# Performance work log

Measured on AMD Instinct MI355X. Metric: run time of the kernel, lower is better.

The kernel has to match this reference:

```python
import jax, jax.numpy as jnp
import numpy as np

B, C, H, W = 8, 256, 64, 64
CR = C // 8  # reduced channels = 32


def setup_inputs() -> dict:
    key = jax.random.key(0)
    k1, k2, k3, k4 = jax.random.split(key, 4)
    x = jax.random.normal(k1, (B, C, H, W), dtype=jnp.float32)
    # 1x1 conv weights (bias=False) are plain channel matmuls; scale like kaiming (~1/sqrt(fan_in))
    Wt = jax.random.normal(k2, (3 * CR, C), dtype=jnp.float32) * (1.0 / np.sqrt(C))
    Wo = jax.random.normal(k3, (C, CR), dtype=jnp.float32) * (1.0 / np.sqrt(CR))
    scale = jax.random.normal(k4, (1,), dtype=jnp.float32)
    return {"x": x, "Wt": Wt, "Wo": Wo, "scale": scale}


def reference(x, Wt, Wo, scale):
    b, c, h, w = x.shape
    n = h * w
    # 1x1 conv QKV projection: [B, 3*Cr, H, W]
    t = jnp.einsum('oc,bchw->bohw', Wt, x)
    cr = t.shape[1] // 3
    key = t[:, :cr].reshape(b, cr, n)          # [B, Cr, N]
    query = t[:, cr:2 * cr].reshape(b, cr, n)  # [B, Cr, N]
    value = t[:, 2 * cr:].reshape(b, cr, n)    # [B, Cr, N]
    # scores[b, i, j] = sum_c key[b,c,i] * query[b,c,j]  (key^T @ query)
    scores = jnp.einsum('bci,bcj->bij', key, query)  # [B, N, N]
    # torch Softmax(dim=1): normalize over the key axis i
    weights = jax.nn.softmax(scores, axis=1)
    # output[b, c, j] = sum_i value[b,c,i] * weights[b,i,j]
    out = jnp.einsum('bci,bij->bcj', value, weights)  # [B, Cr, N]
    out = out.reshape(b, cr, h, w)
    out = jnp.einsum('oc,bchw->bohw', Wo, out)  # 1x1 conv back to C channels
    return scale[0] * out + x
```

## Files before the change

### kernel.cpp

```cpp
#include <hip/hip_runtime.h>
#include <math.h>

#define B_ 8
#define C_ 256
#define CR_ 32
#define N_ 4096
#define NH_ 4

typedef __attribute__((ext_vector_type(8))) short bf16x8;
typedef __attribute__((ext_vector_type(4))) short bf16x4;
typedef __attribute__((ext_vector_type(4))) float f32x4;
typedef __attribute__((ext_vector_type(16))) float f32x16;
typedef __attribute__((ext_vector_type(2))) unsigned uint32x2;

#if defined(__has_builtin)
#if __has_builtin(__builtin_amdgcn_permlane32_swap)
#define HAVE_PLSWAP 1
#endif
#endif

__device__ inline short f2bf(float f) {
  union { float f; unsigned u; } v; v.f = f;
  unsigned r = v.u + 0x7FFFu + ((v.u >> 16) & 1u);
  return (short)(r >> 16);
}
__device__ inline float bf2f(short h) {
  union { unsigned u; float f; } v; v.u = ((unsigned)(unsigned short)h) << 16;
  return v.f;
}
__device__ inline short f2bf_r(float f) {
  return (short)((__float_as_uint(f) + 0x8000u) >> 16);
}


__global__ __launch_bounds__(256) void prep_weights(const float* __restrict__ Wt,
                                                    const float* __restrict__ Wo,
                                                    const float* __restrict__ scale,
                                                    short* __restrict__ WtHi,
                                                    short* __restrict__ WtLo,
                                                    short* __restrict__ WoB) {
  const int blk = blockIdx.x, tid = threadIdx.x;
  if (blk < 96) {
    float v = Wt[blk * C_ + tid];
    if (blk >= 32 && blk < 64) v *= 1.44269504f;
    const short h = f2bf(v);
    WtHi[blk * C_ + tid] = h;
    WtLo[blk * C_ + tid] = f2bf(v - bf2f(h));
  } else {
    const int idx = (blk - 96) * 256 + tid;
    WoB[idx] = f2bf(Wo[idx] * scale[0]);
  }
}

__global__ __launch_bounds__(256) void qkv_mfma(const float* __restrict__ x,
                                                const short* __restrict__ WtHi,
                                                const short* __restrict__ WtLo,
                                                short* __restrict__ Kf,
                                                short* __restrict__ Qf,
                                                short* __restrict__ Vf) {
  const int b = blockIdx.y;
  const int tid = threadIdx.x;
  const int wave = tid >> 6, lane = tid & 63;
  const int col = lane & 15, quad = lane >> 4;
  const int n0 = (blockIdx.x * 4 + wave) * 16;

  const f32x4 z4 = {0.f, 0.f, 0.f, 0.f};
  f32x4 acc[6] = {z4, z4, z4, z4, z4, z4};

  const float* xb = x + (size_t)b * C_ * N_ + n0 + col;
  float xcur[8], xnxt[8];
#pragma unroll
  for (int j = 0; j < 8; ++j) xcur[j] = xb[(size_t)(quad * 8 + j) * N_];

#pragma unroll 2
  for (int c0 = 0; c0 < C_; c0 += 32) {
    if (c0 < C_ - 32) {
#pragma unroll
      for (int j = 0; j < 8; ++j)
        xnxt[j] = xb[(size_t)(c0 + 32 + quad * 8 + j) * N_];
    }
    bf16x8 xh, xl;
#pragma unroll
    for (int j = 0; j < 8; ++j) {
      const short h = (short)(__float_as_uint(xcur[j]) >> 16);
      xh[j] = h;
      xl[j] = f2bf_r(xcur[j] - bf2f(h));
    }
#pragma unroll
    for (int ot = 0; ot < 4; ++ot) {
      const int off = (ot * 16 + col) * C_ + c0 + quad * 8;
      const bf16x8 bh = *(const bf16x8*)(WtHi + off);
      const bf16x8 bl = *(const bf16x8*)(WtLo + off);
      acc[ot] = __builtin_amdgcn_mfma_f32_16x16x32_bf16(xh, bh, acc[ot], 0, 0, 0);
      acc[ot] = __builtin_amdgcn_mfma_f32_16x16x32_bf16(xl, bh, acc[ot], 0, 0, 0);
      acc[ot] = __builtin_amdgcn_mfma_f32_16x16x32_bf16(xh, bl, acc[ot], 0, 0, 0);
    }
#pragma unroll
    for (int ct = 0; ct < 2; ++ct) {
      const int off = ((64 + ct * 16) + col) * C_ + c0 + quad * 8;
      const bf16x8 ah = *(const bf16x8*)(WtHi + off);
      const bf16x8 al = *(const bf16x8*)(WtLo + off);
      acc[4 + ct] = __builtin_amdgcn_mfma_f32_16x16x32_bf16(ah, xh, acc[4 + ct], 0, 0, 0);
      acc[4 + ct] = __builtin_amdgcn_mfma_f32_16x16x32_bf16(ah, xl, acc[4 + ct], 0, 0, 0);
      acc[4 + ct] = __builtin_amdgcn_mfma_f32_16x16x32_bf16(al, xh, acc[4 + ct], 0, 0, 0);
    }
#pragma unroll
    for (int j = 0; j < 8; ++j) xcur[j] = xnxt[j];
  }

#pragma unroll
  for (int ot = 0; ot < 2; ++ot)
#pragma unroll
    for (int r = 0; r < 4; ++r) {
      const int i = n0 + quad * 4 + r;
      const int c = ot * 16 + col;
      const int ln = (i & 31) | (((c >> 3) & 1) << 5);
      Kf[(((size_t)(b * 128 + (i >> 5)) * 2 + (c >> 4)) * 64 + ln) * 8 + (c & 7)] =
          f2bf(acc[ot][r]);
    }
#pragma unroll
  for (int ot = 2; ot < 4; ++ot)
#pragma unroll
    for (int r = 0; r < 4; ++r) {
      const int j = n0 + quad * 4 + r;
      const int c = (ot - 2) * 16 + col;
      const int ln = (j & 31) | (((c >> 3) & 1) << 5);
      Qf[(((size_t)(b * 128 + (j >> 5)) * 2 + (c >> 4)) * 64 + ln) * 8 + (c & 7)] =
          f2bf(acc[ot][r]);
    }
#pragma unroll
  for (int ct = 0; ct < 2; ++ct)
#pragma unroll
    for (int r = 0; r < 4; ++r) {
      const int c = ct * 16 + quad * 4 + r;
      const int n = n0 + col;
      const int ln = c | (((n >> 3) & 1) << 5);
      Vf[((size_t)(b * 256 + (n >> 4)) * 64 + ln) * 8 + (n & 7)] =
          f2bf(acc[4 + ct][r]);
    }
}

__global__ __launch_bounds__(64, 2) void flash_attn(const short* __restrict__ Kf,
                                                    const short* __restrict__ Qf,
                                                    const short* __restrict__ Vf,
                                                    short* __restrict__ OPart,
                                                    float* __restrict__ LPart) {
  const int b = blockIdx.z, hq = blockIdx.y;
  const int jb = blockIdx.x;
  const int lane = threadIdx.x;
  const int j32 = lane & 31, h32 = lane >> 5;

  const f32x16 z16 = {0.f};
  const short* pQ = Qf + ((size_t)(b * 128 + jb * 2) * 2) * 512 + lane * 8;
  bf16x8 qf[2][2];
  qf[0][0] = *(const bf16x8*)(pQ);
  qf[0][1] = *(const bf16x8*)(pQ + 512);
  qf[1][0] = *(const bf16x8*)(pQ + 1024);
  qf[1][1] = *(const bf16x8*)(pQ + 1536);

  const short* pK = Kf + ((size_t)(b * 128 + hq * 32) * 2) * 512 + lane * 8;
  const short* pV = Vf + ((size_t)(b * 256 + hq * 64)) * 512 + lane * 8;

  f32x16 acc[2] = {z16, z16};
  float ps[2] = {0.f, 0.f};

  bf16x8 ka = *(const bf16x8*)(pK);
  bf16x8 kb = *(const bf16x8*)(pK + 512);
  bf16x8 va = *(const bf16x8*)(pV);
  bf16x8 vb = *(const bf16x8*)(pV + 512);

#pragma unroll 1
  for (int t = 0; t < 32; ++t) {
    pK += 1024;
    pV += 1024;
    const bf16x8 kan = *(const bf16x8*)(pK);
    const bf16x8 kbn = *(const bf16x8*)(pK + 512);
    const bf16x8 van = *(const bf16x8*)(pV);
    const bf16x8 vbn = *(const bf16x8*)(pV + 512);

#pragma unroll
    for (int jt = 0; jt < 2; ++jt) {
      __builtin_amdgcn_s_setprio(1);
      f32x16 s = __builtin_amdgcn_mfma_f32_32x32x16_bf16(ka, qf[jt][0], z16, 0, 0, 0);
      s = __builtin_amdgcn_mfma_f32_32x32x16_bf16(kb, qf[jt][1], s, 0, 0, 0);
      __builtin_amdgcn_s_setprio(0);
      float p[16];
#pragma unroll
      for (int r = 0; r < 16; ++r) p[r] = __builtin_amdgcn_exp2f(s[r]);
      ps[jt] += (((p[0] + p[1]) + (p[2] + p[3])) + ((p[4] + p[5]) + (p[6] + p[7]))) +
                (((p[8] + p[9]) + (p[10] + p[11])) + ((p[12] + p[13]) + (p[14] + p[15])));
      unsigned d[8];
#pragma unroll
      for (int k = 0; k < 8; ++k) {
        const unsigned u0 = __float_as_uint(p[2 * k]) + 0x8000u;
        const unsigned u1 = __float_as_uint(p[2 * k + 1]) + 0x8000u;
        d[k] = __builtin_amdgcn_perm(u1, u0, 0x07060302u);
      }
      union { unsigned u[4]; bf16x8 v; } f0, f1;
#ifdef HAVE_PLSWAP
      {
        const uint32x2 r0 = __builtin_amdgcn_permlane32_swap(d[0], d[2], false, false);
        f0.u[0] = r0[0]; f0.u[2] = r0[1];
        const uint32x2 r1 = __builtin_amdgcn_permlane32_swap(d[1], d[3], false, false);
        f0.u[1] = r1[0]; f0.u[3] = r1[1];
        const uint32x2 r2 = __builtin_amdgcn_permlane32_swap(d[4], d[6], false, false);
        f1.u[0] = r2[0]; f1.u[2] = r2[1];
        const uint32x2 r3 = __builtin_amdgcn_permlane32_swap(d[5], d[7], false, false);
        f1.u[1] = r3[0]; f1.u[3] = r3[1];
      }
#else
      {
        unsigned xw[8];
#pragma unroll
        for (int k = 0; k < 8; ++k) xw[k] = __shfl_xor((int)d[k], 32);
        f0.u[0] = h32 ? xw[2] : d[0];
        f0.u[1] = h32 ? xw[3] : d[1];
        f0.u[2] = h32 ? d[2] : xw[0];
        f0.u[3] = h32 ? d[3] : xw[1];
        f1.u[0] = h32 ? xw[6] : d[4];
        f1.u[1] = h32 ? xw[7] : d[5];
        f1.u[2] = h32 ? d[6] : xw[4];
        f1.u[3] = h32 ? d[7] : xw[5];
      }
#endif
      __builtin_amdgcn_s_setprio(1);
      acc[jt] = __builtin_amdgcn_mfma_f32_32x32x16_bf16(va, f0.v, acc[jt], 0, 0, 0);
      acc[jt] = __builtin_amdgcn_mfma_f32_32x32x16_bf16(vb, f1.v, acc[jt], 0, 0, 0);
      __builtin_amdgcn_s_setprio(0);
    }

    ka = kan; kb = kbn; va = van; vb = vbn;
  }

  const size_t base = ((size_t)b * NH_ + hq) * N_;
#pragma unroll
  for (int jt = 0; jt < 2; ++jt) {
    const float l = ps[jt] + __shfl_xor(ps[jt], 32);
    const int jg = (jb * 2 + jt) * 32 + j32;
    if (h32 == 0) LPart[base + jg] = l;
    short* OP = OPart + (base + jg) * 32;
#pragma unroll
    for (int g = 0; g < 4; ++g) {
      bf16x4 o = {f2bf(acc[jt][4 * g + 0]), f2bf(acc[jt][4 * g + 1]),
                  f2bf(acc[jt][4 * g + 2]), f2bf(acc[jt][4 * g + 3])};
      *(bf16x4*)(OP + 8 * g + 4 * h32) = o;
    }
  }
}

__global__ __launch_bounds__(256) void out_proj(const short* __restrict__ OPart,
                                                const float* __restrict__ LPart,
                                                const short* __restrict__ WoB,
                                                const float* __restrict__ x,
                                                float* __restrict__ out) {
  const int b = blockIdx.z, chalf = blockIdx.y;
  const int tid = threadIdx.x;
  const int wave = tid >> 6, lane = tid & 63;
  const int col = lane & 15, quad = lane >> 4;
  const int jg = blockIdx.x * 64 + wave * 16 + col;
  const int n0 = blockIdx.x * 64 + wave * 16;

  float osum[8];
#pragma unroll
  for (int e = 0; e < 8; ++e) osum[e] = 0.f;
  float lsum = 0.f;
#pragma unroll
  for (int h = 0; h < NH_; ++h) {
    const size_t p = ((size_t)b * NH_ + h) * N_ + jg;
    const bf16x8 o = *(const bf16x8*)(OPart + p * 32 + quad * 8);
#pragma unroll
    for (int e = 0; e < 8; ++e) osum[e] += bf2f(o[e]);
    lsum += LPart[p];
  }
  const float linv = 1.f / lsum;
  bf16x8 bf;
#pragma unroll
  for (int e = 0; e < 8; ++e) bf[e] = f2bf(osum[e] * linv);

  const f32x4 z4 = {0.f, 0.f, 0.f, 0.f};
  const float* xb = x + (size_t)b * C_ * N_;
  float* ob = out + (size_t)b * C_ * N_;
#pragma unroll
  for (int ct = 0; ct < 8; ++ct) {
    const int ctg = chalf * 8 + ct;
    const bf16x8 af = *(const bf16x8*)(WoB + (ctg * 16 + col) * 32 + quad * 8);
    const f32x4 a = __builtin_amdgcn_mfma_f32_16x16x32_bf16(af, bf, z4, 0, 0, 0);
#pragma unroll
    for (int r = 0; r < 4; ++r) {
      const size_t idx = (size_t)(ctg * 16 + quad * 4 + r) * N_ + n0 + col;
      ob[idx] = a[r] + xb[idx];
    }
  }
}

extern "C" void kernel_launch(void* const* d_in, const int* in_sizes, int n_in,
                              void* d_out, int out_size, void* d_ws,
                              size_t ws_size, hipStream_t stream) {
  const float* x = (const float*)d_in[0];
  const float* Wt = (const float*)d_in[1];
  const float* Wo = (const float*)d_in[2];
  const float* scale = (const float*)d_in[3];
  float* out = (float*)d_out;

  short* OPart = (short*)d_ws;
  float* LPart = (float*)(OPart + (size_t)B_ * NH_ * N_ * 32);
  short* Kf = (short*)(LPart + (size_t)B_ * NH_ * N_);
  short* Qf = Kf + (size_t)B_ * 128 * 1024;
  short* Vf = Qf + (size_t)B_ * 128 * 1024;
  short* WtHi = Vf + (size_t)B_ * 256 * 512;
  short* WtLo = WtHi + 96 * C_;
  short* WoB = WtLo + 96 * C_;

  prep_weights<<<dim3(128), 256, 0, stream>>>(Wt, Wo, scale, WtHi, WtLo, WoB);
  qkv_mfma<<<dim3(64, B_), 256, 0, stream>>>(x, WtHi, WtLo, Kf, Qf, Vf);
  flash_attn<<<dim3(64, NH_, B_), 64, 0, stream>>>(Kf, Qf, Vf, OPart, LPart);
  out_proj<<<dim3(64, 2, B_), 256, 0, stream>>>(OPart, LPart, WoB, x, out);
}
```

Baseline: 152.2 us.

## Remap attention blocks per XCD and deepen K/V prefetch to two tiles

Flattens the flash_attn grid to 1D and remaps block IDs so each XCD (round-robin block dispatch across 8 XCDs) handles the same batch/head groups. The intent is for blocks sharing K/V to hit the same L2. It also unrolls the key loop by two and prefetches K/V two tiles ahead, to hide global load latency. This raises register pressure under launch_bounds(64,2).

```diff
diff --git a/kernel.cpp b/kernel.cpp
--- a/kernel.cpp
+++ b/kernel.cpp
@@ -145,8 +145,11 @@
                                                     const short* __restrict__ Vf,
                                                     short* __restrict__ OPart,
                                                     float* __restrict__ LPart) {
-  const int b = blockIdx.z, hq = blockIdx.y;
-  const int jb = blockIdx.x;
+  const int bid = blockIdx.x;
+  const int xcd = bid & 7, w = bid >> 3;
+  const int g = xcd * 4 + (w >> 6);
+  const int b = g >> 2, hq = g & 3;
+  const int jb = w & 63;
   const int lane = threadIdx.x;
   const int j32 = lane & 31, h32 = lane >> 5;
 
@@ -164,20 +167,17 @@
   f32x16 acc[2] = {z16, z16};
   float ps[2] = {0.f, 0.f};
 
-  bf16x8 ka = *(const bf16x8*)(pK);
-  bf16x8 kb = *(const bf16x8*)(pK + 512);
-  bf16x8 va = *(const bf16x8*)(pV);
-  bf16x8 vb = *(const bf16x8*)(pV + 512);
-
-#pragma unroll 1
-  for (int t = 0; t < 32; ++t) {
-    pK += 1024;
-    pV += 1024;
-    const bf16x8 kan = *(const bf16x8*)(pK);
-    const bf16x8 kbn = *(const bf16x8*)(pK + 512);
-    const bf16x8 van = *(const bf16x8*)(pV);
-    const bf16x8 vbn = *(const bf16x8*)(pV + 512);
-
+  bf16x8 ka0 = *(const bf16x8*)(pK);
+  bf16x8 kb0 = *(const bf16x8*)(pK + 512);
+  bf16x8 va0 = *(const bf16x8*)(pV);
+  bf16x8 vb0 = *(const bf16x8*)(pV + 512);
+  bf16x8 ka1 = *(const bf16x8*)(pK + 1024);
+  bf16x8 kb1 = *(const bf16x8*)(pK + 1536);
+  bf16x8 va1 = *(const bf16x8*)(pV + 1024);
+  bf16x8 vb1 = *(const bf16x8*)(pV + 1536);
+
+  auto tile_step = [&](const bf16x8& ka, const bf16x8& kb,
+                       const bf16x8& va, const bf16x8& vb) {
 #pragma unroll
     for (int jt = 0; jt < 2; ++jt) {
       __builtin_amdgcn_s_setprio(1);
@@ -228,8 +228,24 @@
       acc[jt] = __builtin_amdgcn_mfma_f32_32x32x16_bf16(vb, f1.v, acc[jt], 0, 0, 0);
       __builtin_amdgcn_s_setprio(0);
     }
-
-    ka = kan; kb = kbn; va = van; vb = vbn;
+  };
+
+#pragma unroll 1
+  for (int t = 0; t < 32; t += 2) {
+    const bf16x8 ka2 = *(const bf16x8*)(pK + 2048);
+    const bf16x8 kb2 = *(const bf16x8*)(pK + 2560);
+    const bf16x8 va2 = *(const bf16x8*)(pV + 2048);
+    const bf16x8 vb2 = *(const bf16x8*)(pV + 2560);
+    tile_step(ka0, kb0, va0, vb0);
+    const bf16x8 ka3 = *(const bf16x8*)(pK + 3072);
+    const bf16x8 kb3 = *(const bf16x8*)(pK + 3584);
+    const bf16x8 va3 = *(const bf16x8*)(pV + 3072);
+    const bf16x8 vb3 = *(const bf16x8*)(pV + 3584);
+    tile_step(ka1, kb1, va1, vb1);
+    ka0 = ka2; kb0 = kb2; va0 = va2; vb0 = vb2;
+    ka1 = ka3; kb1 = kb3; va1 = va3; vb1 = vb3;
+    pK += 2048;
+    pV += 2048;
   }
 
   const size_t base = ((size_t)b * NH_ + hq) * N_;
@@ -240,10 +256,10 @@
     if (h32 == 0) LPart[base + jg] = l;
     short* OP = OPart + (base + jg) * 32;
 #pragma unroll
-    for (int g = 0; g < 4; ++g) {
-      bf16x4 o = {f2bf(acc[jt][4 * g + 0]), f2bf(acc[jt][4 * g + 1]),
-                  f2bf(acc[jt][4 * g + 2]), f2bf(acc[jt][4 * g + 3])};
-      *(bf16x4*)(OP + 8 * g + 4 * h32) = o;
+    for (int g2 = 0; g2 < 4; ++g2) {
+      bf16x4 o = {f2bf(acc[jt][4 * g2 + 0]), f2bf(acc[jt][4 * g2 + 1]),
+                  f2bf(acc[jt][4 * g2 + 2]), f2bf(acc[jt][4 * g2 + 3])};
+      *(bf16x4*)(OP + 8 * g2 + 4 * h32) = o;
     }
   }
 }
@@ -313,6 +329,6 @@
 
   prep_weights<<<dim3(128), 256, 0, stream>>>(Wt, Wo, scale, WtHi, WtLo, WoB);
   qkv_mfma<<<dim3(64, B_), 256, 0, stream>>>(x, WtHi, WtLo, Kf, Qf, Vf);
-  flash_attn<<<dim3(64, NH_, B_), 64, 0, stream>>>(Kf, Qf, Vf, OPart, LPart);
+  flash_attn<<<dim3(2048), 64, 0, stream>>>(Kf, Qf, Vf, OPart, LPart);
   out_proj<<<dim3(64, 2, B_), 256, 0, stream>>>(OPart, LPart, WoB, x, out);
 }
```

Result: no change. 150.7 us (-1.0%).

## Split attention keys eight ways, remap blocks per XCD, use packed bf16 convert

Applied to the files above, without the earlier changes.

Doubles the key-axis split from 4 to 8 partial chunks, so each flash_attn block walks 16 key tiles instead of 32 and the grid becomes a flat 4096 blocks. A manual blockIdx swizzle keeps each batch/head group on one XCD for L2 locality. Occupancy hint is raised to 4 waves per SIMD, V loads are no longer double-buffered, and the manual bf16 rounding is replaced by v_cvt_pk_bf16_f32 inline asm. The cost is twice as many partial outputs for out_proj to reduce, plus possible exposed V load latency.

```diff
diff --git a/kernel.cpp b/kernel.cpp
--- a/kernel.cpp
+++ b/kernel.cpp
@@ -5,7 +5,7 @@
 #define C_ 256
 #define CR_ 32
 #define N_ 4096
-#define NH_ 4
+#define NH_ 8
 
 typedef __attribute__((ext_vector_type(8))) short bf16x8;
 typedef __attribute__((ext_vector_type(4))) short bf16x4;
@@ -30,6 +30,12 @@
 }
 __device__ inline short f2bf_r(float f) {
   return (short)((__float_as_uint(f) + 0x8000u) >> 16);
+}
+
+__device__ inline unsigned cvt_pk_bf16(float a, float b) {
+  unsigned d;
+  asm("v_cvt_pk_bf16_f32 %0, %1, %2" : "=v"(d) : "v"(a), "v"(b));
+  return d;
 }
 
 
@@ -140,13 +146,16 @@
     }
 }
 
-__global__ __launch_bounds__(64, 2) void flash_attn(const short* __restrict__ Kf,
+__global__ __launch_bounds__(64, 4) void flash_attn(const short* __restrict__ Kf,
                                                     const short* __restrict__ Qf,
                                                     const short* __restrict__ Vf,
                                                     short* __restrict__ OPart,
                                                     float* __restrict__ LPart) {
-  const int b = blockIdx.z, hq = blockIdx.y;
-  const int jb = blockIdx.x;
+  const int bid = blockIdx.x;
+  const int xcd = bid & 7, w = bid >> 3;
+  const int g = xcd * 8 + (w >> 6);
+  const int b = g >> 3, hq = g & 7;
+  const int jb = w & 63;
   const int lane = threadIdx.x;
   const int j32 = lane & 31, h32 = lane >> 5;
 
@@ -158,25 +167,23 @@
   qf[1][0] = *(const bf16x8*)(pQ + 1024);
   qf[1][1] = *(const bf16x8*)(pQ + 1536);
 
-  const short* pK = Kf + ((size_t)(b * 128 + hq * 32) * 2) * 512 + lane * 8;
-  const short* pV = Vf + ((size_t)(b * 256 + hq * 64)) * 512 + lane * 8;
+  const short* pK = Kf + ((size_t)(b * 128 + hq * 16) * 2) * 512 + lane * 8;
+  const short* pV = Vf + ((size_t)(b * 256 + hq * 32)) * 512 + lane * 8;
 
   f32x16 acc[2] = {z16, z16};
   float ps[2] = {0.f, 0.f};
 
   bf16x8 ka = *(const bf16x8*)(pK);
   bf16x8 kb = *(const bf16x8*)(pK + 512);
-  bf16x8 va = *(const bf16x8*)(pV);
-  bf16x8 vb = *(const bf16x8*)(pV + 512);
 
 #pragma unroll 1
-  for (int t = 0; t < 32; ++t) {
+  for (int t = 0; t < 16; ++t) {
+    const bf16x8 va = *(const bf16x8*)(pV);
+    const bf16x8 vb = *(const bf16x8*)(pV + 512);
     pK += 1024;
     pV += 1024;
     const bf16x8 kan = *(const bf16x8*)(pK);
     const bf16x8 kbn = *(const bf16x8*)(pK + 512);
-    const bf16x8 van = *(const bf16x8*)(pV);
-    const bf16x8 vbn = *(const bf16x8*)(pV + 512);
 
 #pragma unroll
     for (int jt = 0; jt < 2; ++jt) {
@@ -189,28 +196,31 @@
       for (int r = 0; r < 16; ++r) p[r] = __builtin_amdgcn_exp2f(s[r]);
       ps[jt] += (((p[0] + p[1]) + (p[2] + p[3])) + ((p[4] + p[5]) + (p[6] + p[7]))) +
                 (((p[8] + p[9]) + (p[10] + p[11])) + ((p[12] + p[13]) + (p[14] + p[15])));
-      unsigned d[8];
-#pragma unroll
-      for (int k = 0; k < 8; ++k) {
-        const unsigned u0 = __float_as_uint(p[2 * k]) + 0x8000u;
-        const unsigned u1 = __float_as_uint(p[2 * k + 1]) + 0x8000u;
-        d[k] = __builtin_amdgcn_perm(u1, u0, 0x07060302u);
-      }
       union { unsigned u[4]; bf16x8 v; } f0, f1;
 #ifdef HAVE_PLSWAP
       {
-        const uint32x2 r0 = __builtin_amdgcn_permlane32_swap(d[0], d[2], false, false);
+        const unsigned d0 = cvt_pk_bf16(p[0], p[1]);
+        const unsigned d1 = cvt_pk_bf16(p[2], p[3]);
+        const unsigned d2 = cvt_pk_bf16(p[4], p[5]);
+        const unsigned d3 = cvt_pk_bf16(p[6], p[7]);
+        const uint32x2 r0 = __builtin_amdgcn_permlane32_swap(d0, d2, false, false);
         f0.u[0] = r0[0]; f0.u[2] = r0[1];
-        const uint32x2 r1 = __builtin_amdgcn_permlane32_swap(d[1], d[3], false, false);
+        const uint32x2 r1 = __builtin_amdgcn_permlane32_swap(d1, d3, false, false);
         f0.u[1] = r1[0]; f0.u[3] = r1[1];
-        const uint32x2 r2 = __builtin_amdgcn_permlane32_swap(d[4], d[6], false, false);
+        const unsigned d4 = cvt_pk_bf16(p[8], p[9]);
+        const unsigned d5 = cvt_pk_bf16(p[10], p[11]);
+        const unsigned d6 = cvt_pk_bf16(p[12], p[13]);
+        const unsigned d7 = cvt_pk_bf16(p[14], p[15]);
+        const uint32x2 r2 = __builtin_amdgcn_permlane32_swap(d4, d6, false, false);
         f1.u[0] = r2[0]; f1.u[2] = r2[1];
-        const uint32x2 r3 = __builtin_amdgcn_permlane32_swap(d[5], d[7], false, false);
+        const uint32x2 r3 = __builtin_amdgcn_permlane32_swap(d5, d7, false, false);
         f1.u[1] = r3[0]; f1.u[3] = r3[1];
       }
 #else
       {
-        unsigned xw[8];
+        unsigned d[8], xw[8];
+#pragma unroll
+        for (int k = 0; k < 8; ++k) d[k] = cvt_pk_bf16(p[2 * k], p[2 * k + 1]);
 #pragma unroll
         for (int k = 0; k < 8; ++k) xw[k] = __shfl_xor((int)d[k], 32);
         f0.u[0] = h32 ? xw[2] : d[0];
@@ -228,8 +238,8 @@
       acc[jt] = __builtin_amdgcn_mfma_f32_32x32x16_bf16(vb, f1.v, acc[jt], 0, 0, 0);
       __builtin_amdgcn_s_setprio(0);
     }
-
-    ka = kan; kb = kbn; va = van; vb = vbn;
+    ka = kan;
+    kb = kbn;
   }
 
   const size_t base = ((size_t)b * NH_ + hq) * N_;
@@ -240,10 +250,10 @@
     if (h32 == 0) LPart[base + jg] = l;
     short* OP = OPart + (base + jg) * 32;
 #pragma unroll
-    for (int g = 0; g < 4; ++g) {
-      bf16x4 o = {f2bf(acc[jt][4 * g + 0]), f2bf(acc[jt][4 * g + 1]),
-                  f2bf(acc[jt][4 * g + 2]), f2bf(acc[jt][4 * g + 3])};
-      *(bf16x4*)(OP + 8 * g + 4 * h32) = o;
+    for (int g2 = 0; g2 < 4; ++g2) {
+      bf16x4 o = {f2bf(acc[jt][4 * g2 + 0]), f2bf(acc[jt][4 * g2 + 1]),
+                  f2bf(acc[jt][4 * g2 + 2]), f2bf(acc[jt][4 * g2 + 3])};
+      *(bf16x4*)(OP + 8 * g2 + 4 * h32) = o;
     }
   }
 }
@@ -313,6 +323,6 @@
 
   prep_weights<<<dim3(128), 256, 0, stream>>>(Wt, Wo, scale, WtHi, WtLo, WoB);
   qkv_mfma<<<dim3(64, B_), 256, 0, stream>>>(x, WtHi, WtLo, Kf, Qf, Vf);
-  flash_attn<<<dim3(64, NH_, B_), 64, 0, stream>>>(Kf, Qf, Vf, OPart, LPart);
+  flash_attn<<<dim3(4096), 64, 0, stream>>>(Kf, Qf, Vf, OPart, LPart);
   out_proj<<<dim3(64, 2, B_), 256, 0, stream>>>(OPart, LPart, WoB, x, out);
 }
```

Result: no change. 152.5 us (+0.2%).
